# Performance work log

Hardware: AMD Instinct MI355X
Metric: run time of the kernel (lower is better)

Reference implementation:

```python
import jax, jax.numpy as jnp
import numpy as np

HEADSIZE = 64  # Attention 'channels' arg: per-head dim used by split_heads and the scale


def setup_inputs() -> dict:
    key = jax.random.key(0)
    # [B, C, T, H, W]; C must equal channels*heads = 512 (channel_split constraint)
    x = jax.random.normal(key, (4, 512, 8, 14, 14), dtype=jnp.float32)
    return {"x": x}


def _attention(x):
    # qkv = SplitIdentity(3): repeat along channels then split back -> q = k = v = x
    B, C, T, H, W = x.shape
    N = T * H * W
    # Tokenizer.tokenize with token_dim=None: permute(0, T, H, W, C) -> [B, N, C]
    tok = jnp.transpose(x, (0, 2, 3, 4, 1)).reshape(B, N, C)
    # split_heads: reshape(B, N, headsize, heads).permute(0, 3, 1, 2) -> [B, h, N, d]
    q = tok.reshape(B, N, HEADSIZE, -1).transpose(0, 3, 1, 2)
    # qkv_aggregate: double scaling (q*s) @ (k^T * s), softmax, @ v ; s = d**-0.5
    scale = HEADSIZE ** -0.5
    scores = jnp.einsum('bhnd,bhmd->bhnm', q * scale, q * scale)  # [B,h,N,N]
    attn = jax.nn.softmax(scores, axis=-1)
    out = jnp.einsum('bhnm,bhmd->bhnd', attn, q)
    # merge_heads: permute(0, 2, 3, 1).reshape(B, N, d*h) — inverse of split_heads
    merged = out.transpose(0, 2, 3, 1).reshape(B, N, C)
    # untokenize: [B, T, H, W, C] -> [B, C, T, H, W]; proj = identity, dropouts p=0
    return merged.reshape(B, T, H, W, C).transpose(0, 4, 1, 2, 3)


def reference(x):
    return _attention(x)
```

## Files before the change

### kernel.cpp

```cpp
#include <hip/hip_runtime.h>

typedef _Float16 f16x8 __attribute__((ext_vector_type(8)));
typedef _Float16 f16x4 __attribute__((ext_vector_type(4)));
typedef float    f32x4 __attribute__((ext_vector_type(4)));
typedef unsigned int u32x4 __attribute__((ext_vector_type(4)));

constexpr int NTOK   = 1568;
constexpr int NHEADS = 8;
constexpr int NCH    = 512;
constexpr int NC32   = 52;
constexpr float SK   = 0.15014030f;
constexpr size_t IMG_BH = (size_t)NC32 * 4096;

__global__ __launch_bounds__(256)
void prep_kernel(const float* __restrict__ x, char* __restrict__ Kimg, char* __restrict__ Vimg)
{
    const int bh = blockIdx.x, c32 = blockIdx.y;
    const int b = bh >> 3, h = bh & 7;
    const int t = threadIdx.x;
    const int f = t >> 6, l = t & 63, l15 = l & 15, grp = l >> 4;

    char* Kg = Kimg + (size_t)bh * IMG_BH + (size_t)(c32 * 4 + f) * 1024 + l * 16;
    char* Vg = Vimg + (size_t)bh * IMG_BH + (size_t)(c32 * 4 + f) * 1024 + l * 16;

    const int n0 = c32 * 32;
    if (n0 >= NTOK) {
        f16x8 z;
#pragma unroll
        for (int j = 0; j < 8; ++j) z[j] = (_Float16)0.f;
        *(f16x8*)Kg = z; *(f16x8*)Vg = z;
        return;
    }

    __shared__ _Float16 kbuf[32][72];
    __shared__ _Float16 vbuf[64][40];

    const int tok = t & 31, dhi = t >> 5;
#pragma unroll
    for (int p = 0; p < 8; ++p) {
        const int d = 8 * p + dhi;
        const float v = x[((size_t)b * NCH + d * NHEADS + h) * NTOK + n0 + tok];
        kbuf[tok][d] = (_Float16)(v * SK);
        vbuf[d][tok] = (_Float16)v;
    }
    __syncthreads();

    *(f16x8*)Kg = *(const f16x8*)&kbuf[(f >> 1) * 16 + l15][(f & 1) * 32 + grp * 8];
    f16x4 va = *(const f16x4*)&vbuf[f * 16 + l15][4 * grp];
    f16x4 vb = *(const f16x4*)&vbuf[f * 16 + l15][16 + 4 * grp];
    f16x8 vv;
#pragma unroll
    for (int j = 0; j < 4; ++j) { vv[j] = va[j]; vv[4 + j] = vb[j]; }
    *(f16x8*)Vg = vv;
}

static __device__ __forceinline__ f16x8 make_bp(f32x4 sA, f32x4 sB)
{
    u32x4 w;
    w[0] = __builtin_bit_cast(unsigned int,
        __builtin_amdgcn_cvt_pkrtz(__builtin_amdgcn_exp2f(sA[0]), __builtin_amdgcn_exp2f(sA[1])));
    w[1] = __builtin_bit_cast(unsigned int,
        __builtin_amdgcn_cvt_pkrtz(__builtin_amdgcn_exp2f(sA[2]), __builtin_amdgcn_exp2f(sA[3])));
    w[2] = __builtin_bit_cast(unsigned int,
        __builtin_amdgcn_cvt_pkrtz(__builtin_amdgcn_exp2f(sB[0]), __builtin_amdgcn_exp2f(sB[1])));
    w[3] = __builtin_bit_cast(unsigned int,
        __builtin_amdgcn_cvt_pkrtz(__builtin_amdgcn_exp2f(sB[2]), __builtin_amdgcn_exp2f(sB[3])));
    return __builtin_bit_cast(f16x8, w);
}

static __device__ __forceinline__ void load4(const char* base,
                                             f16x8& f0, f16x8& f1, f16x8& f2, f16x8& f3)
{
    f0 = *(const f16x8*)(base);
    f1 = *(const f16x8*)(base + 1024);
    f2 = *(const f16x8*)(base + 2048);
    f3 = *(const f16x8*)(base + 3072);
}

static __device__ __forceinline__ void chunk_compute(
    const f16x8& k0, const f16x8& k1, const f16x8& k2, const f16x8& k3,
    const f16x8& v0, const f16x8& v1, const f16x8& v2, const f16x8& v3,
    const f16x8 (&aq)[2][2], const f16x8& ones,
    f32x4 (&oacc)[2][4], f32x4 (&lacc)[2])
{
    const f32x4 z4 = {0.f, 0.f, 0.f, 0.f};
#pragma unroll
    for (int sub = 0; sub < 2; ++sub) {
        f32x4 sA = __builtin_amdgcn_mfma_f32_16x16x32_f16(k0, aq[sub][0], z4, 0, 0, 0);
        sA = __builtin_amdgcn_mfma_f32_16x16x32_f16(k1, aq[sub][1], sA, 0, 0, 0);
        f32x4 sB = __builtin_amdgcn_mfma_f32_16x16x32_f16(k2, aq[sub][0], z4, 0, 0, 0);
        sB = __builtin_amdgcn_mfma_f32_16x16x32_f16(k3, aq[sub][1], sB, 0, 0, 0);
        const f16x8 bp = make_bp(sA, sB);
        lacc[sub]   = __builtin_amdgcn_mfma_f32_16x16x32_f16(ones, bp, lacc[sub], 0, 0, 0);
        oacc[sub][0] = __builtin_amdgcn_mfma_f32_16x16x32_f16(v0, bp, oacc[sub][0], 0, 0, 0);
        oacc[sub][1] = __builtin_amdgcn_mfma_f32_16x16x32_f16(v1, bp, oacc[sub][1], 0, 0, 0);
        oacc[sub][2] = __builtin_amdgcn_mfma_f32_16x16x32_f16(v2, bp, oacc[sub][2], 0, 0, 0);
        oacc[sub][3] = __builtin_amdgcn_mfma_f32_16x16x32_f16(v3, bp, oacc[sub][3], 0, 0, 0);
    }
}

static __device__ __forceinline__ void dump_part(float (*row)[35], int lane,
                                                 const f32x4 (&oacc)[2][4], const f32x4 (&lacc)[2])
{
#pragma unroll
    for (int s = 0; s < 2; ++s) {
#pragma unroll
        for (int db = 0; db < 4; ++db)
#pragma unroll
            for (int q = 0; q < 4; ++q) row[lane][s * 16 + db * 4 + q] = oacc[s][db][q];
        row[lane][32 + s] = lacc[s][0];
    }
}
static __device__ __forceinline__ void add_part(const float (*row)[35], int lane,
                                                f32x4 (&oacc)[2][4], f32x4 (&lacc)[2])
{
#pragma unroll
    for (int s = 0; s < 2; ++s) {
#pragma unroll
        for (int db = 0; db < 4; ++db)
#pragma unroll
            for (int q = 0; q < 4; ++q) oacc[s][db][q] += row[lane][s * 16 + db * 4 + q];
        lacc[s][0] += row[lane][32 + s];
    }
}

__global__ __launch_bounds__(256, 3)
void attn_fwd(const char* __restrict__ Kimg, const char* __restrict__ Vimg,
              float* __restrict__ out)
{
    const int orig = blockIdx.x;
    const int wgid = (orig & 7) * 196 + (orig >> 3);
    const int qt = wgid % 49, bh = wgid / 49;
    const int b = bh >> 3, head = bh & 7;
    const int t = threadIdx.x, kw = t >> 6, lane = t & 63;
    const int l15 = lane & 15, grp = lane >> 4;

    const char* Kb = Kimg + (size_t)bh * IMG_BH;
    const char* Vb = Vimg + (size_t)bh * IMG_BH;

    f16x8 aq[2][2];
#pragma unroll
    for (int sub = 0; sub < 2; ++sub)
#pragma unroll
        for (int ks = 0; ks < 2; ++ks)
            aq[sub][ks] = *(const f16x8*)(Kb + (size_t)((qt * 2 + sub) * 2 + ks) * 1024 + lane * 16);

    f16x8 ones;
#pragma unroll
    for (int j = 0; j < 8; ++j) ones[j] = (_Float16)1.f;

    f32x4 oacc[2][4];
    f32x4 lacc[2];
#pragma unroll
    for (int s = 0; s < 2; ++s) {
        lacc[s] = f32x4{0.f, 0.f, 0.f, 0.f};
#pragma unroll
        for (int db = 0; db < 4; ++db) oacc[s][db] = f32x4{0.f, 0.f, 0.f, 0.f};
    }

    const int start = (kw == 0) ? 0 : 13 + (kw - 1) * 12;
    const int nc    = (kw == 0) ? 13 : 12;

    f16x8 ak0, ak1, ak2, ak3, av0, av1, av2, av3;
    f16x8 bk0, bk1, bk2, bk3, bv0, bv1, bv2, bv3;

    load4(Kb + (size_t)start * 4096 + lane * 16, ak0, ak1, ak2, ak3);
    load4(Vb + (size_t)start * 4096 + lane * 16, av0, av1, av2, av3);

    int i = 0;
    for (; i + 2 <= nc; i += 2) {
        load4(Kb + (size_t)(start + i + 1) * 4096 + lane * 16, bk0, bk1, bk2, bk3);
        load4(Vb + (size_t)(start + i + 1) * 4096 + lane * 16, bv0, bv1, bv2, bv3);
        chunk_compute(ak0, ak1, ak2, ak3, av0, av1, av2, av3, aq, ones, oacc, lacc);
        load4(Kb + (size_t)(start + i + 2) * 4096 + lane * 16, ak0, ak1, ak2, ak3);
        load4(Vb + (size_t)(start + i + 2) * 4096 + lane * 16, av0, av1, av2, av3);
        chunk_compute(bk0, bk1, bk2, bk3, bv0, bv1, bv2, bv3, aq, ones, oacc, lacc);
    }
    if (i < nc)
        chunk_compute(ak0, ak1, ak2, ak3, av0, av1, av2, av3, aq, ones, oacc, lacc);

    __shared__ float comb[64][35];
    for (int r = 1; r < 4; ++r) {
        if (kw == r) dump_part(comb, lane, oacc, lacc);
        __syncthreads();
        if (kw == 0) add_part(comb, lane, oacc, lacc);
        __syncthreads();
    }

    if (kw == 0) {
#pragma unroll
        for (int sub = 0; sub < 2; ++sub) {
            const int qrow = qt * 32 + sub * 16 + l15;
            const float inv = 1.0f / lacc[sub][0];
#pragma unroll
            for (int db = 0; db < 4; ++db)
#pragma unroll
                for (int q = 0; q < 4; ++q) {
                    const int d = db * 16 + 4 * grp + q;
                    out[((size_t)b * NCH + (size_t)d * NHEADS + head) * NTOK + qrow] = oacc[sub][db][q] * inv;
                }
        }
    }
}

extern "C" void kernel_launch(void* const* d_in, const int* in_sizes, int n_in,
                              void* d_out, int out_size, void* d_ws, size_t ws_size,
                              hipStream_t stream)
{
    const float* x = (const float*)d_in[0];
    float* out     = (float*)d_out;

    char* Kimg = (char*)d_ws;
    char* Vimg = (char*)d_ws + 32 * IMG_BH;

    dim3 pgrid(32, NC32);
    prep_kernel<<<pgrid, 256, 0, stream>>>(x, Kimg, Vimg);

    attn_fwd<<<1568, 256, 0, stream>>>(Kimg, Vimg, out);
}
```

Measured before the change: 43.99 us.

## Share K/V chunks across four query waves via double-buffered LDS

Each workgroup now handles 128 query rows, one 32-row slice per wave, instead of splitting one 32-row tile's keys across waves. K/V chunks are staged once into double-buffered shared memory and read by all four waves. This removes the cross-wave partial-sum reduction and cuts global K/V traffic by sharing loads. In exchange there is a block barrier per chunk, the grid is smaller (416 blocks), and padded query tiles at the end waste some compute.

```diff
diff --git a/kernel.cpp b/kernel.cpp
--- a/kernel.cpp
+++ b/kernel.cpp
@@ -68,15 +68,6 @@
     return __builtin_bit_cast(f16x8, w);
 }
 
-static __device__ __forceinline__ void load4(const char* base,
-                                             f16x8& f0, f16x8& f1, f16x8& f2, f16x8& f3)
-{
-    f0 = *(const f16x8*)(base);
-    f1 = *(const f16x8*)(base + 1024);
-    f2 = *(const f16x8*)(base + 2048);
-    f3 = *(const f16x8*)(base + 3072);
-}
-
 static __device__ __forceinline__ void chunk_compute(
     const f16x8& k0, const f16x8& k1, const f16x8& k2, const f16x8& k3,
     const f16x8& v0, const f16x8& v1, const f16x8& v2, const f16x8& v3,
@@ -91,36 +82,11 @@
         f32x4 sB = __builtin_amdgcn_mfma_f32_16x16x32_f16(k2, aq[sub][0], z4, 0, 0, 0);
         sB = __builtin_amdgcn_mfma_f32_16x16x32_f16(k3, aq[sub][1], sB, 0, 0, 0);
         const f16x8 bp = make_bp(sA, sB);
-        lacc[sub]   = __builtin_amdgcn_mfma_f32_16x16x32_f16(ones, bp, lacc[sub], 0, 0, 0);
+        lacc[sub]    = __builtin_amdgcn_mfma_f32_16x16x32_f16(ones, bp, lacc[sub], 0, 0, 0);
         oacc[sub][0] = __builtin_amdgcn_mfma_f32_16x16x32_f16(v0, bp, oacc[sub][0], 0, 0, 0);
         oacc[sub][1] = __builtin_amdgcn_mfma_f32_16x16x32_f16(v1, bp, oacc[sub][1], 0, 0, 0);
         oacc[sub][2] = __builtin_amdgcn_mfma_f32_16x16x32_f16(v2, bp, oacc[sub][2], 0, 0, 0);
         oacc[sub][3] = __builtin_amdgcn_mfma_f32_16x16x32_f16(v3, bp, oacc[sub][3], 0, 0, 0);
-    }
-}
-
-static __device__ __forceinline__ void dump_part(float (*row)[35], int lane,
-                                                 const f32x4 (&oacc)[2][4], const f32x4 (&lacc)[2])
-{
-#pragma unroll
-    for (int s = 0; s < 2; ++s) {
-#pragma unroll
-        for (int db = 0; db < 4; ++db)
-#pragma unroll
-            for (int q = 0; q < 4; ++q) row[lane][s * 16 + db * 4 + q] = oacc[s][db][q];
-        row[lane][32 + s] = lacc[s][0];
-    }
-}
-static __device__ __forceinline__ void add_part(const float (*row)[35], int lane,
-                                                f32x4 (&oacc)[2][4], f32x4 (&lacc)[2])
-{
-#pragma unroll
-    for (int s = 0; s < 2; ++s) {
-#pragma unroll
-        for (int db = 0; db < 4; ++db)
-#pragma unroll
-            for (int q = 0; q < 4; ++q) oacc[s][db][q] += row[lane][s * 16 + db * 4 + q];
-        lacc[s][0] += row[lane][32 + s];
     }
 }
 
@@ -129,11 +95,14 @@
               float* __restrict__ out)
 {
     const int orig = blockIdx.x;
-    const int wgid = (orig & 7) * 196 + (orig >> 3);
-    const int qt = wgid % 49, bh = wgid / 49;
+    const int wgid = (orig & 7) * 52 + (orig >> 3);
+    const int qt = wgid % 13, bh = wgid / 13;
     const int b = bh >> 3, head = bh & 7;
-    const int t = threadIdx.x, kw = t >> 6, lane = t & 63;
+    const int t = threadIdx.x, wave = t >> 6, lane = t & 63;
     const int l15 = lane & 15, grp = lane >> 4;
+
+    __shared__ __align__(16) char kls[2][4096];
+    __shared__ __align__(16) char vls[2][4096];
 
     const char* Kb = Kimg + (size_t)bh * IMG_BH;
     const char* Vb = Vimg + (size_t)bh * IMG_BH;
@@ -143,7 +112,7 @@
     for (int sub = 0; sub < 2; ++sub)
 #pragma unroll
         for (int ks = 0; ks < 2; ++ks)
-            aq[sub][ks] = *(const f16x8*)(Kb + (size_t)((qt * 2 + sub) * 2 + ks) * 1024 + lane * 16);
+            aq[sub][ks] = *(const f16x8*)(Kb + (size_t)((qt * 8 + wave * 2 + sub) * 2 + ks) * 1024 + lane * 16);
 
     f16x8 ones;
 #pragma unroll
@@ -158,39 +127,42 @@
         for (int db = 0; db < 4; ++db) oacc[s][db] = f32x4{0.f, 0.f, 0.f, 0.f};
     }
 
-    const int start = (kw == 0) ? 0 : 13 + (kw - 1) * 12;
-    const int nc    = (kw == 0) ? 13 : 12;
+    const int soff = t * 16;
 
-    f16x8 ak0, ak1, ak2, ak3, av0, av1, av2, av3;
-    f16x8 bk0, bk1, bk2, bk3, bv0, bv1, bv2, bv3;
+    {
+        f16x8 sk = *(const f16x8*)(Kb + soff);
+        f16x8 sv = *(const f16x8*)(Vb + soff);
+        *(f16x8*)&kls[0][soff] = sk;
+        *(f16x8*)&vls[0][soff] = sv;
+    }
+    __syncthreads();
 
-    load4(Kb + (size_t)start * 4096 + lane * 16, ak0, ak1, ak2, ak3);
-    load4(Vb + (size_t)start * 4096 + lane * 16, av0, av1, av2, av3);
+    for (int c = 0; c < 49; ++c) {
+        const int cur = c & 1, nxt = cur ^ 1;
 
-    int i = 0;
-    for (; i + 2 <= nc; i += 2) {
-        load4(Kb + (size_t)(start + i + 1) * 4096 + lane * 16, bk0, bk1, bk2, bk3);
-        load4(Vb + (size_t)(start + i + 1) * 4096 + lane * 16, bv0, bv1, bv2, bv3);
-        chunk_compute(ak0, ak1, ak2, ak3, av0, av1, av2, av3, aq, ones, oacc, lacc);
-        load4(Kb + (size_t)(start + i + 2) * 4096 + lane * 16, ak0, ak1, ak2, ak3);
-        load4(Vb + (size_t)(start + i + 2) * 4096 + lane * 16, av0, av1, av2, av3);
-        chunk_compute(bk0, bk1, bk2, bk3, bv0, bv1, bv2, bv3, aq, ones, oacc, lacc);
-    }
-    if (i < nc)
-        chunk_compute(ak0, ak1, ak2, ak3, av0, av1, av2, av3, aq, ones, oacc, lacc);
+        f16x8 sk = *(const f16x8*)(Kb + (size_t)(c + 1) * 4096 + soff);
+        f16x8 sv = *(const f16x8*)(Vb + (size_t)(c + 1) * 4096 + soff);
 
-    __shared__ float comb[64][35];
-    for (int r = 1; r < 4; ++r) {
-        if (kw == r) dump_part(comb, lane, oacc, lacc);
-        __syncthreads();
-        if (kw == 0) add_part(comb, lane, oacc, lacc);
+        f16x8 k0 = *(const f16x8*)&kls[cur][lane * 16];
+        f16x8 k1 = *(const f16x8*)&kls[cur][1024 + lane * 16];
+        f16x8 k2 = *(const f16x8*)&kls[cur][2048 + lane * 16];
+        f16x8 k3 = *(const f16x8*)&kls[cur][3072 + lane * 16];
+        f16x8 v0 = *(const f16x8*)&vls[cur][lane * 16];
+        f16x8 v1 = *(const f16x8*)&vls[cur][1024 + lane * 16];
+        f16x8 v2 = *(const f16x8*)&vls[cur][2048 + lane * 16];
+        f16x8 v3 = *(const f16x8*)&vls[cur][3072 + lane * 16];
+        chunk_compute(k0, k1, k2, k3, v0, v1, v2, v3, aq, ones, oacc, lacc);
+
+        *(f16x8*)&kls[nxt][soff] = sk;
+        *(f16x8*)&vls[nxt][soff] = sv;
         __syncthreads();
     }
 
-    if (kw == 0) {
 #pragma unroll
-        for (int sub = 0; sub < 2; ++sub) {
-            const int qrow = qt * 32 + sub * 16 + l15;
+    for (int sub = 0; sub < 2; ++sub) {
+        const int s16 = qt * 8 + wave * 2 + sub;
+        if (s16 < 98) {
+            const int qrow = s16 * 16 + l15;
             const float inv = 1.0f / lacc[sub][0];
 #pragma unroll
             for (int db = 0; db < 4; ++db)
@@ -216,5 +188,5 @@
     dim3 pgrid(32, NC32);
     prep_kernel<<<pgrid, 256, 0, stream>>>(x, Kimg, Vimg);
 
-    attn_fwd<<<1568, 256, 0, stream>>>(Kimg, Vimg, out);
+    attn_fwd<<<416, 256, 0, stream>>>(Kimg, Vimg, out);
 }
```

New measurement: 44.85 us. Within noise of the previous version (+2.0%).
